# Performance work log

Measured on AMD Instinct MI355X. Metric: run time of the kernel, lower is better.

The kernel has to match this reference:

```python
import jax, jax.numpy as jnp
import numpy as np

D_MODEL = 768
N_HEAD = 12
HEAD_DIM = D_MODEL // N_HEAD
D_FF = 4 * D_MODEL
EPS = 1e-5


def setup_inputs() -> dict:
    key = jax.random.key(0)
    ks = jax.random.split(key, 12)
    B, S = 4, 1024
    s = 0.02
    return {
        "x": jax.random.normal(ks[0], (B, S, D_MODEL), jnp.float32),
        "ln1_g": jnp.ones((D_MODEL,), jnp.float32),
        "ln1_b": jnp.zeros((D_MODEL,), jnp.float32),
        "ln2_g": jnp.ones((D_MODEL,), jnp.float32),
        "ln2_b": jnp.zeros((D_MODEL,), jnp.float32),
        "w_attn": jax.random.normal(ks[1], (D_MODEL, 3 * D_MODEL), jnp.float32) * s,
        "b_attn": jnp.zeros((3 * D_MODEL,), jnp.float32),
        "w_proj": jax.random.normal(ks[2], (D_MODEL, D_MODEL), jnp.float32) * s,
        "b_proj": jnp.zeros((D_MODEL,), jnp.float32),
        "w_fc": jax.random.normal(ks[3], (D_MODEL, D_FF), jnp.float32) * s,
        "b_fc": jnp.zeros((D_FF,), jnp.float32),
        "w_mlp_proj": jax.random.normal(ks[4], (D_FF, D_MODEL), jnp.float32) * s,
        "b_mlp_proj": jnpp.zeros((D_MODEL,), jnp.float32) if False else jnp.zeros((D_MODEL,), jnp.float32),
    }


def layer_norm(x, g, b):
    mu = jnp.mean(x, axis=-1, keepdims=True)
    var = jnp.mean(jnp.square(x - mu), axis=-1, keepdims=True)
    return (x - mu) * jax.lax.rsqrt(var + EPS) * g + b


def attention(x, w_attn, b_attn, w_proj, b_proj):
    B, S, _ = x.shape
    qkv = x @ w_attn + b_attn                      # [B,S,3D]
    q, k, v = jnp.split(qkv, 3, axis=-1)
    def heads(t):
        return t.reshape(B, S, N_HEAD, HEAD_DIM).transpose(0, 2, 1, 3)  # [B,H,S,hd]
    q, k, v = heads(q), heads(k), heads(v)
    scale = HEAD_DIM ** (-0.5)
    att = jnp.einsum("bhqd,bhkd->bhqk", q, k) * scale
    # additive causal mask: strictly-upper triangle gets -1e9 (matches TF source)
    mask = 1.0 - jnp.tril(jnp.ones((S, S), att.dtype))
    att = att + mask * (-1e9)
    att = jax.nn.softmax(att, axis=-1)
    y = jnp.einsum("bhqk,bhkd->bhqd", att, v)
    y = y.transpose(0, 2, 1, 3).reshape(B, S, D_MODEL)
    return y @ w_proj + b_proj


def mlp(x, w_fc, b_fc, w_mlp_proj, b_mlp_proj):
    h = jax.nn.gelu(x @ w_fc + b_fc, approximate=True)
    return h @ w_mlp_proj + b_mlp_proj


def reference(x, ln1_g, ln1_b, ln2_g, ln2_b, w_attn, b_attn, w_proj, b_proj,
              w_fc, b_fc, w_mlp_proj, b_mlp_proj):
    x = x + attention(layer_norm(x, ln1_g, ln1_b), w_attn, b_attn, w_proj, b_proj)
    x = x + mlp(layer_norm(x, ln2_g, ln2_b), w_fc, b_fc, w_mlp_proj, b_mlp_proj)
    return x
```

## Files before the change

### kernel.cpp

```cpp
#include <hip/hip_runtime.h>

typedef unsigned short u16;
typedef short bf8_t __attribute__((ext_vector_type(8)));
typedef float f32x4 __attribute__((ext_vector_type(4)));

__device__ __forceinline__ u16 f2bf(float f) {
  unsigned u = __builtin_bit_cast(unsigned, f);
  unsigned r = (u + 0x7fffu + ((u >> 16) & 1u)) >> 16;
  return (u16)r;
}

__device__ __forceinline__ void gld16(const void* g, void* l) {
  __builtin_amdgcn_global_load_lds((const __attribute__((address_space(1))) unsigned int*)g,
                                   (__attribute__((address_space(3))) unsigned int*)l, 16, 0, 0);
}

#define MFMA(a, b, c) __builtin_amdgcn_mfma_f32_16x16x32_bf16((a), (b), (c), 0, 0, 0)

__global__ void wtrans_kernel(const float* __restrict__ W, u16* __restrict__ WT, int K, int N) {
  __shared__ float tile[32][33];
  const int n0 = blockIdx.x << 5, k0 = blockIdx.y << 5;
  const int tx = threadIdx.x, ty = threadIdx.y;
#pragma unroll
  for (int i = 0; i < 4; i++) {
    const int r = ty + (i << 3);
    tile[r][tx] = W[(size_t)(k0 + r) * N + n0 + tx];
  }
  __syncthreads();
#pragma unroll
  for (int i = 0; i < 4; i++) {
    const int r = ty + (i << 3);
    WT[(size_t)(n0 + r) * K + k0 + tx] = f2bf(tile[tx][r]);
  }
}

__global__ void ln_kernel(const float* __restrict__ x, const float* __restrict__ g,
                          const float* __restrict__ bb, u16* __restrict__ o) {
  const int row = blockIdx.x, t = threadIdx.x;
  const float* xr = x + (size_t)row * 768;
  float v[3];
#pragma unroll
  for (int i = 0; i < 3; i++) v[i] = xr[t + (i << 8)];
  float s = v[0] + v[1] + v[2];
#pragma unroll
  for (int off = 1; off < 64; off <<= 1) s += __shfl_xor(s, off, 64);
  __shared__ float red[4];
  const int w = t >> 6;
  if ((t & 63) == 0) red[w] = s;
  __syncthreads();
  const float mu = (red[0] + red[1] + red[2] + red[3]) * (1.f / 768.f);
  float q = 0.f;
#pragma unroll
  for (int i = 0; i < 3; i++) {
    v[i] -= mu;
    q += v[i] * v[i];
  }
#pragma unroll
  for (int off = 1; off < 64; off <<= 1) q += __shfl_xor(q, off, 64);
  __syncthreads();
  if ((t & 63) == 0) red[w] = q;
  __syncthreads();
  const float var = (red[0] + red[1] + red[2] + red[3]) * (1.f / 768.f);
  const float rs = rsqrtf(var + 1e-5f);
#pragma unroll
  for (int i = 0; i < 3; i++) {
    const int idx = t + (i << 8);
    o[(size_t)row * 768 + idx] = f2bf(v[i] * rs * g[idx] + bb[idx]);
  }
}

template <int EPI>
__global__ void gemm_kernel(const u16* __restrict__ A, const u16* __restrict__ BT,
                            const float* __restrict__ bias, const float* __restrict__ res,
                            void* __restrict__ outp, int M, int N, int K) {
  __shared__ __align__(16) u16 As[128 * 32];
  __shared__ __align__(16) u16 Bs[128 * 32];
  const int m0 = blockIdx.y << 7, n0 = blockIdx.x << 7;
  const int tid = threadIdx.x, lane = tid & 63, w = tid >> 6;
  const int wr = w >> 1, wc = w & 1;
  const int l16 = lane & 15, kg = lane >> 4;
  f32x4 acc[4][4];
  const f32x4 fz = {0.f, 0.f, 0.f, 0.f};
#pragma unroll
  for (int i = 0; i < 4; i++)
#pragma unroll
    for (int j = 0; j < 4; j++) acc[i][j] = fz;

  const int c1 = (w << 6) + lane;
  const int r1 = c1 >> 2, ko1 = (c1 & 3) << 3;
  const int c2 = c1 + 256;
  const int r2 = c2 >> 2, ko2 = (c2 & 3) << 3;
  const int nkt = K >> 5;
  for (int kt = 0; kt < nkt; kt++) {
    const int k0 = kt << 5;
    __syncthreads();
    gld16(A + (size_t)(m0 + r1) * K + k0 + ko1, As + (size_t)(c1 - lane) * 8);
    gld16(A + (size_t)(m0 + r2) * K + k0 + ko2, As + (size_t)(c2 - lane) * 8);
    gld16(BT + (size_t)(n0 + r1) * K + k0 + ko1, Bs + (size_t)(c1 - lane) * 8);
    gld16(BT + (size_t)(n0 + r2) * K + k0 + ko2, Bs + (size_t)(c2 - lane) * 8);
    __syncthreads();
    bf8_t af[4], bfr[4];
#pragma unroll
    for (int mf = 0; mf < 4; mf++)
      af[mf] = *(const bf8_t*)&As[((wr << 6) + (mf << 4) + l16) * 32 + (kg << 3)];
#pragma unroll
    for (int nf = 0; nf < 4; nf++)
      bfr[nf] = *(const bf8_t*)&Bs[((wc << 6) + (nf << 4) + l16) * 32 + (kg << 3)];
#pragma unroll
    for (int mf = 0; mf < 4; mf++)
#pragma unroll
      for (int nf = 0; nf < 4; nf++) acc[mf][nf] = MFMA(af[mf], bfr[nf], acc[mf][nf]);
  }
#pragma unroll
  for (int mf = 0; mf < 4; mf++) {
#pragma unroll
    for (int nf = 0; nf < 4; nf++) {
      const int col = n0 + (wc << 6) + (nf << 4) + l16;
      const float bv = bias[col];
#pragma unroll
      for (int j = 0; j < 4; j++) {
        const int row = m0 + (wr << 6) + (mf << 4) + (kg << 2) + j;
        float v = acc[mf][nf][j] + bv;
        if constexpr (EPI == 0) {
          ((u16*)outp)[(size_t)row * N + col] = f2bf(v);
        } else if constexpr (EPI == 1) {
          const float u = 0.7978845608f * (v + 0.044715f * v * v * v);
          const float e = __expf(2.f * u);
          const float th = 1.f - 2.f / (e + 1.f);
          ((u16*)outp)[(size_t)row * N + col] = f2bf(0.5f * v * (1.f + th));
        } else {
          v += res[(size_t)row * N + col];
          ((float*)outp)[(size_t)row * N + col] = v;
        }
      }
    }
  }
}

__global__ void attn_kernel(const u16* __restrict__ qkv, u16* __restrict__ y) {
  __shared__ __align__(16) u16 Qs[64 * 64];
  __shared__ __align__(16) u16 Ks[2][64 * 64];
  __shared__ __align__(16) u16 Vt[2][64 * 64];
  __shared__ __align__(16) u16 Ps[4][16 * 72];
  const int qt = (int)gridDim.x - 1 - (int)blockIdx.x;
  const int bh = blockIdx.y;
  const int b = bh / 12, h = bh - b * 12;
  const size_t brow = (size_t)b << 10;
  const int q0 = qt << 6;
  const int tid = threadIdx.x, lane = tid & 63, w = tid >> 6;
  const int l16 = lane & 15, kg = lane >> 4;

  const int c1 = tid, c2 = tid + 256;
  const int row1 = c1 >> 3, cc1 = c1 & 7;
  const int row2 = c2 >> 3, cc2 = c2 & 7;
  const int sw1 = ((cc1 ^ (row1 & 7)) << 3);
  const int sw2 = ((cc2 ^ (row2 & 7)) << 3);
  const int sg1 = ((cc1 & 1) << 2) | (cc1 & 2) | ((cc1 >> 2) & 1);
  const int sg2 = ((cc2 & 1) << 2) | (cc2 & 2) | ((cc2 >> 2) & 1);
  const int vcol1 = row1 ^ (sg1 << 3), d01 = cc1 << 3;
  const int vcol2 = row2 ^ (sg2 << 3), d02 = cc2 << 3;

  const int cbQ = h << 6, cbK = 768 + (h << 6), cbV = 1536 + (h << 6);

  gld16(qkv + (brow + q0 + row1) * 2304 + cbQ + sw1, Qs + (size_t)(c1 - lane) * 8);
  gld16(qkv + (brow + q0 + row2) * 2304 + cbQ + sw2, Qs + (size_t)(c2 - lane) * 8);
  gld16(qkv + (brow + row1) * 2304 + cbK + sw1, Ks[0] + (size_t)(c1 - lane) * 8);
  gld16(qkv + (brow + row2) * 2304 + cbK + sw2, Ks[0] + (size_t)(c2 - lane) * 8);
  bf8_t v1 = *(const bf8_t*)(qkv + (brow + row1) * 2304 + cbV + (cc1 << 3));
  bf8_t v2 = *(const bf8_t*)(qkv + (brow + row2) * 2304 + cbV + (cc2 << 3));

  bf8_t qf[2];
  f32x4 oacc[4];
  const f32x4 fz = {0.f, 0.f, 0.f, 0.f};
#pragma unroll
  for (int dg = 0; dg < 4; dg++) oacc[dg] = fz;
  float mrun[4], lrun[4];
#pragma unroll
  for (int j = 0; j < 4; j++) {
    mrun[j] = -1e30f;
    lrun[j] = 0.f;
  }

  for (int kt = 0; kt <= qt; kt++) {
    const int cur = kt & 1;
    u16* Vc = Vt[cur];
#pragma unroll
    for (int i = 0; i < 8; i++) Vc[(d01 + i) * 64 + vcol1] = (u16)v1[i];
#pragma unroll
    for (int i = 0; i < 8; i++) Vc[(d02 + i) * 64 + vcol2] = (u16)v2[i];
    __syncthreads();

    if (kt == 0) {
      const int qrow = (w << 4) + l16;
#pragma unroll
      for (int hd = 0; hd < 2; hd++) {
        const int ch = (kg + (hd << 2)) ^ (qrow & 7);
        qf[hd] = *(const bf8_t*)&Qs[qrow * 64 + (ch << 3)];
      }
    }
    if (kt < qt) {
      const int nr = (kt + 1) << 6;
      gld16(qkv + (brow + nr + row1) * 2304 + cbK + sw1, Ks[cur ^ 1] + (size_t)(c1 - lane) * 8);
      gld16(qkv + (brow + nr + row2) * 2304 + cbK + sw2, Ks[cur ^ 1] + (size_t)(c2 - lane) * 8);
      v1 = *(const bf8_t*)(qkv + (brow + nr + row1) * 2304 + cbV + (cc1 << 3));
      v2 = *(const bf8_t*)(qkv + (brow + nr + row2) * 2304 + cbV + (cc2 << 3));
    }

    const u16* Kc = Ks[cur];
    float sv[4][4];
#pragma unroll
    for (int g = 0; g < 4; g++) {
      f32x4 z = fz;
      const int key = (g << 4) + l16;
#pragma unroll
      for (int hd = 0; hd < 2; hd++) {
        const int ch = (kg + (hd << 2)) ^ (key & 7);
        const bf8_t kf = *(const bf8_t*)&Kc[key * 64 + (ch << 3)];
        z = MFMA(qf[hd], kf, z);
      }
      const int gkey = (kt << 6) + key;
#pragma unroll
      for (int j = 0; j < 4; j++) {
        const int grow = q0 + (w << 4) + (kg << 2) + j;
        sv[g][j] = (gkey <= grow) ? z[j] * 0.125f : -1e30f;
      }
    }
    float tm[4];
#pragma unroll
    for (int j = 0; j < 4; j++)
      tm[j] = fmaxf(fmaxf(sv[0][j], sv[1][j]), fmaxf(sv[2][j], sv[3][j]));
#pragma unroll
    for (int o = 1; o < 16; o <<= 1)
#pragma unroll
      for (int j = 0; j < 4; j++) tm[j] = fmaxf(tm[j], __shfl_xor(tm[j], o, 64));
    float corr[4], tsum[4];
#pragma unroll
    for (int j = 0; j < 4; j++) {
      const float mn = fmaxf(mrun[j], tm[j]);
      corr[j] = __expf(mrun[j] - mn);
      mrun[j] = mn;
      tsum[j] = 0.f;
    }
#pragma unroll
    for (int g = 0; g < 4; g++)
#pragma unroll
      for (int j = 0; j < 4; j++) {
        const float p = __expf(sv[g][j] - mrun[j]);
        sv[g][j] = p;
        tsum[j] += p;
      }
#pragma unroll
    for (int o = 1; o < 16; o <<= 1)
#pragma unroll
      for (int j = 0; j < 4; j++) tsum[j] += __shfl_xor(tsum[j], o, 64);
#pragma unroll
    for (int j = 0; j < 4; j++) lrun[j] = lrun[j] * corr[j] + tsum[j];
#pragma unroll
    for (int dg = 0; dg < 4; dg++)
#pragma unroll
      for (int j = 0; j < 4; j++) oacc[dg][j] *= corr[j];
#pragma unroll
    for (int g = 0; g < 4; g++)
#pragma unroll
      for (int j = 0; j < 4; j++)
        Ps[w][((kg << 2) + j) * 72 + (g << 4) + l16] = f2bf(sv[g][j]);
    bf8_t pf[2];
#pragma unroll
    for (int kh = 0; kh < 2; kh++)
      pf[kh] = *(const bf8_t*)&Ps[w][l16 * 72 + (kg << 3) + (kh << 5)];
#pragma unroll
    for (int dg = 0; dg < 4; dg++) {
      const int sgr = (((l16 >> 3) & 1) << 2) | ((dg & 1) << 1) | (dg >> 1);
      const int d = (dg << 4) + l16;
#pragma unroll
      for (int kh = 0; kh < 2; kh++) {
        const bf8_t vf = *(const bf8_t*)&Vc[d * 64 + ((((kh << 2) + kg) ^ sgr) << 3)];
        oacc[dg] = MFMA(pf[kh], vf, oacc[dg]);
      }
    }
  }
  float inv[4];
#pragma unroll
  for (int j = 0; j < 4; j++) inv[j] = 1.f / lrun[j];
#pragma unroll
  for (int dg = 0; dg < 4; dg++)
#pragma unroll
    for (int j = 0; j < 4; j++) {
      const size_t grow = brow + q0 + (w << 4) + (kg << 2) + j;
      y[grow * 768 + (h << 6) + (dg << 4) + l16] = f2bf(oacc[dg][j] * inv[j]);
    }
}

extern "C" void kernel_launch(void* const* d_in, const int* in_sizes, int n_in,
                              void* d_out, int out_size, void* d_ws, size_t ws_size,
                              hipStream_t stream) {
  const float* x = (const float*)d_in[0];
  const float* ln1_g = (const float*)d_in[1];
  const float* ln1_b = (const float*)d_in[2];
  const float* ln2_g = (const float*)d_in[3];
  const float* ln2_b = (const float*)d_in[4];
  const float* w_attn = (const float*)d_in[5];
  const float* b_attn = (const float*)d_in[6];
  const float* w_proj = (const float*)d_in[7];
  const float* b_proj = (const float*)d_in[8];
  const float* w_fc = (const float*)d_in[9];
  const float* b_fc = (const float*)d_in[10];
  const float* w_mlp = (const float*)d_in[11];
  const float* b_mlp = (const float*)d_in[12];
  float* out = (float*)d_out;

  char* ws = (char*)d_ws;
  u16* wqkvT = (u16*)(ws + 0);
  u16* wprojT = (u16*)(ws + 3538944);
  u16* wfcT = (u16*)(ws + 4718592);
  u16* wmlpT = (u16*)(ws + 9437184);
  u16* xn = (u16*)(ws + 14155776);
  u16* qkv = (u16*)(ws + 20447232);
  u16* hbuf = (u16*)(ws + 20447232);
  u16* yb = (u16*)(ws + 45613056);
  float* x1 = (float*)(ws + 51904512);

  const dim3 wtb(32, 8);
  wtrans_kernel<<<dim3(2304 / 32, 768 / 32), wtb, 0, stream>>>(w_attn, wqkvT, 768, 2304);
  wtrans_kernel<<<dim3(768 / 32, 768 / 32), wtb, 0, stream>>>(w_proj, wprojT, 768, 768);
  wtrans_kernel<<<dim3(3072 / 32, 768 / 32), wtb, 0, stream>>>(w_fc, wfcT, 768, 3072);
  wtrans_kernel<<<dim3(768 / 32, 3072 / 32), wtb, 0, stream>>>(w_mlp, wmlpT, 3072, 768);

  ln_kernel<<<4096, 256, 0, stream>>>(x, ln1_g, ln1_b, xn);
  gemm_kernel<0><<<dim3(2304 / 128, 4096 / 128), 256, 0, stream>>>(xn, wqkvT, b_attn, nullptr,
                                                                   qkv, 4096, 2304, 768);
  attn_kernel<<<dim3(16, 48), 256, 0, stream>>>(qkv, yb);
  gemm_kernel<2><<<dim3(768 / 128, 4096 / 128), 256, 0, stream>>>(yb, wprojT, b_proj, x, x1,
                                                                  4096, 768, 768);
  ln_kernel<<<4096, 256, 0, stream>>>(x1, ln2_g, ln2_b, xn);
  gemm_kernel<1><<<dim3(3072 / 128, 4096 / 128), 256, 0, stream>>>(xn, wfcT, b_fc, nullptr,
                                                                   hbuf, 4096, 3072, 768);
  gemm_kernel<2><<<dim3(768 / 128, 4096 / 128), 256, 0, stream>>>(hbuf, wmlpT, b_mlp, x1, out,
                                                                  4096, 768, 3072);
}
```

Measured before the change: 229.5 us.

## Double-buffer GEMM LDS tiles and split-K the narrow projection GEMMs

The GEMM kernel now double-buffers its A/B shared-memory tiles, so the next k-tile's global-to-LDS loads are issued before the current tile's MFMAs, dropping one barrier per iteration. The two N=768 GEMMs (attention projection and MLP down-projection) launch only 192 blocks, which leaves many CUs idle. They are now split along K into 2 or 4 partial-sum slabs (when the workspace is large enough), and a separate reduce kernel adds the slabs, the bias and the residual. This costs extra fp32 partial-buffer traffic and one more launch per GEMM in exchange for more parallelism and load/compute overlap.

```diff
diff --git a/kernel.cpp b/kernel.cpp
--- a/kernel.cpp
+++ b/kernel.cpp
@@ -72,10 +72,11 @@
 template <int EPI>
 __global__ void gemm_kernel(const u16* __restrict__ A, const u16* __restrict__ BT,
                             const float* __restrict__ bias, const float* __restrict__ res,
-                            void* __restrict__ outp, int M, int N, int K) {
-  __shared__ __align__(16) u16 As[128 * 32];
-  __shared__ __align__(16) u16 Bs[128 * 32];
+                            void* __restrict__ outp, int M, int N, int K, int kLen) {
+  __shared__ __align__(16) u16 As[2][128 * 32];
+  __shared__ __align__(16) u16 Bs[2][128 * 32];
   const int m0 = blockIdx.y << 7, n0 = blockIdx.x << 7;
+  const int kOff = blockIdx.z * kLen;
   const int tid = threadIdx.x, lane = tid & 63, w = tid >> 6;
   const int wr = w >> 1, wc = w & 1;
   const int l16 = lane & 15, kg = lane >> 4;
@@ -90,33 +91,41 @@
   const int r1 = c1 >> 2, ko1 = (c1 & 3) << 3;
   const int c2 = c1 + 256;
   const int r2 = c2 >> 2, ko2 = (c2 & 3) << 3;
-  const int nkt = K >> 5;
+  const int lb1 = (c1 - lane) * 8, lb2 = (c2 - lane) * 8;
+
+  auto stage = [&](int buf, int kt) {
+    const int k0 = kOff + (kt << 5);
+    gld16(A + (size_t)(m0 + r1) * K + k0 + ko1, As[buf] + lb1);
+    gld16(A + (size_t)(m0 + r2) * K + k0 + ko2, As[buf] + lb2);
+    gld16(BT + (size_t)(n0 + r1) * K + k0 + ko1, Bs[buf] + lb1);
+    gld16(BT + (size_t)(n0 + r2) * K + k0 + ko2, Bs[buf] + lb2);
+  };
+
+  const int nkt = kLen >> 5;
+  stage(0, 0);
   for (int kt = 0; kt < nkt; kt++) {
-    const int k0 = kt << 5;
+    const int cur = kt & 1;
     __syncthreads();
-    gld16(A + (size_t)(m0 + r1) * K + k0 + ko1, As + (size_t)(c1 - lane) * 8);
-    gld16(A + (size_t)(m0 + r2) * K + k0 + ko2, As + (size_t)(c2 - lane) * 8);
-    gld16(BT + (size_t)(n0 + r1) * K + k0 + ko1, Bs + (size_t)(c1 - lane) * 8);
-    gld16(BT + (size_t)(n0 + r2) * K + k0 + ko2, Bs + (size_t)(c2 - lane) * 8);
-    __syncthreads();
+    if (kt + 1 < nkt) stage(cur ^ 1, kt + 1);
     bf8_t af[4], bfr[4];
 #pragma unroll
     for (int mf = 0; mf < 4; mf++)
-      af[mf] = *(const bf8_t*)&As[((wr << 6) + (mf << 4) + l16) * 32 + (kg << 3)];
+      af[mf] = *(const bf8_t*)&As[cur][((wr << 6) + (mf << 4) + l16) * 32 + (kg << 3)];
 #pragma unroll
     for (int nf = 0; nf < 4; nf++)
-      bfr[nf] = *(const bf8_t*)&Bs[((wc << 6) + (nf << 4) + l16) * 32 + (kg << 3)];
+      bfr[nf] = *(const bf8_t*)&Bs[cur][((wc << 6) + (nf << 4) + l16) * 32 + (kg << 3)];
 #pragma unroll
     for (int mf = 0; mf < 4; mf++)
 #pragma unroll
       for (int nf = 0; nf < 4; nf++) acc[mf][nf] = MFMA(af[mf], bfr[nf], acc[mf][nf]);
   }
+  float* pout = (float*)outp + (size_t)blockIdx.z * M * N;
 #pragma unroll
   for (int mf = 0; mf < 4; mf++) {
 #pragma unroll
     for (int nf = 0; nf < 4; nf++) {
       const int col = n0 + (wc << 6) + (nf << 4) + l16;
-      const float bv = bias[col];
+      const float bv = (EPI == 3) ? 0.f : bias[col];
 #pragma unroll
       for (int j = 0; j < 4; j++) {
         const int row = m0 + (wr << 6) + (mf << 4) + (kg << 2) + j;
@@ -128,13 +137,26 @@
           const float e = __expf(2.f * u);
           const float th = 1.f - 2.f / (e + 1.f);
           ((u16*)outp)[(size_t)row * N + col] = f2bf(0.5f * v * (1.f + th));
-        } else {
+        } else if constexpr (EPI == 2) {
           v += res[(size_t)row * N + col];
           ((float*)outp)[(size_t)row * N + col] = v;
+        } else {
+          pout[(size_t)row * N + col] = v;
         }
       }
     }
   }
+}
+
+__global__ void reduce_kernel(const float* __restrict__ parts, const float* __restrict__ bias,
+                              const float* __restrict__ res, float* __restrict__ out, int ns) {
+  const int row = blockIdx.x, col = threadIdx.x << 2;
+  const size_t base = (size_t)row * 768 + col;
+  f32x4 a = *(const f32x4*)(parts + base);
+  for (int s = 1; s < ns; s++) a += *(const f32x4*)(parts + (size_t)s * 4096 * 768 + base);
+  const f32x4 bv = *(const f32x4*)(bias + col);
+  const f32x4 rv = *(const f32x4*)(res + base);
+  *(f32x4*)(out + base) = a + bv + rv;
 }
 
 __global__ void attn_kernel(const u16* __restrict__ qkv, u16* __restrict__ y) {
@@ -319,6 +341,11 @@
   u16* hbuf = (u16*)(ws + 20447232);
   u16* yb = (u16*)(ws + 45613056);
   float* x1 = (float*)(ws + 51904512);
+  float* parts = (float*)(ws + 64487424);
+
+  const size_t PSZ = (size_t)4096 * 768 * 4;
+  const int nsMlp = (ws_size >= 64487424 + 4 * PSZ) ? 4 : (ws_size >= 64487424 + 2 * PSZ ? 2 : 1);
+  const int nsProj = (ws_size >= 64487424 + 2 * PSZ) ? 2 : 1;
 
   const dim3 wtb(32, 8);
   wtrans_kernel<<<dim3(2304 / 32, 768 / 32), wtb, 0, stream>>>(w_attn, wqkvT, 768, 2304);
@@ -327,14 +354,29 @@
   wtrans_kernel<<<dim3(768 / 32, 3072 / 32), wtb, 0, stream>>>(w_mlp, wmlpT, 3072, 768);
 
   ln_kernel<<<4096, 256, 0, stream>>>(x, ln1_g, ln1_b, xn);
-  gemm_kernel<0><<<dim3(2304 / 128, 4096 / 128), 256, 0, stream>>>(xn, wqkvT, b_attn, nullptr,
-                                                                   qkv, 4096, 2304, 768);
+  gemm_kernel<0><<<dim3(18, 32), 256, 0, stream>>>(xn, wqkvT, b_attn, nullptr, qkv,
+                                                   4096, 2304, 768, 768);
   attn_kernel<<<dim3(16, 48), 256, 0, stream>>>(qkv, yb);
-  gemm_kernel<2><<<dim3(768 / 128, 4096 / 128), 256, 0, stream>>>(yb, wprojT, b_proj, x, x1,
-                                                                  4096, 768, 768);
+
+  if (nsProj == 2) {
+    gemm_kernel<3><<<dim3(6, 32, 2), 256, 0, stream>>>(yb, wprojT, nullptr, nullptr, parts,
+                                                       4096, 768, 768, 384);
+    reduce_kernel<<<4096, 192, 0, stream>>>(parts, b_proj, x, x1, 2);
+  } else {
+    gemm_kernel<2><<<dim3(6, 32), 256, 0, stream>>>(yb, wprojT, b_proj, x, x1,
+                                                    4096, 768, 768, 768);
+  }
+
   ln_kernel<<<4096, 256, 0, stream>>>(x1, ln2_g, ln2_b, xn);
-  gemm_kernel<1><<<dim3(3072 / 128, 4096 / 128), 256, 0, stream>>>(xn, wfcT, b_fc, nullptr,
-                                                                   hbuf, 4096, 3072, 768);
-  gemm_kernel<2><<<dim3(768 / 128, 4096 / 128), 256, 0, stream>>>(hbuf, wmlpT, b_mlp, x1, out,
-                                                                  4096, 768, 3072);
-}
+  gemm_kernel<1><<<dim3(24, 32), 256, 0, stream>>>(xn, wfcT, b_fc, nullptr, hbuf,
+                                                   4096, 3072, 768, 768);
+
+  if (nsMlp > 1) {
+    gemm_kernel<3><<<dim3(6, 32, nsMlp), 256, 0, stream>>>(hbuf, wmlpT, nullptr, nullptr, parts,
+                                                           4096, 768, 3072, 3072 / nsMlp);
+    reduce_kernel<<<4096, 192, 0, stream>>>(parts, b_mlp, x1, out, nsMlp);
+  } else {
+    gemm_kernel<2><<<dim3(6, 32), 256, 0, stream>>>(hbuf, wmlpT, b_mlp, x1, out,
+                                                    4096, 768, 3072, 3072);
+  }
+}
```

After: 213.9 us. 1.07x faster.
